# Kernel tuning notes

Hardware: AMD Instinct MI355X
Metric: run time of the kernel (lower is better)

## Reference

```python
import jax, jax.numpy as jnp
import numpy as np

B, N, D, DK = 8, 2048, 1024, 64
GAMMA = 0.001

def setup_inputs() -> dict:
    key = jax.random.key(0)
    ks = jax.random.split(key, 6)
    x = jax.random.normal(ks[0], (B, N, D), dtype=jnp.float32)
    # nn.Linear weights are [out_features, in_features]; init std=gamma,
    # except fc1/fc2 (modules 4,5) which get std=1e-12 in the original.
    Wq = GAMMA * jax.random.normal(ks[1], (DK, D), dtype=jnp.float32)
    Wk = GAMMA * jax.random.normal(ks[2], (DK, D), dtype=jnp.float32)
    Wv = GAMMA * jax.random.normal(ks[3], (D, D), dtype=jnp.float32)
    W1 = 1e-12 * jax.random.normal(ks[4], (DK, D), dtype=jnp.float32)
    W2 = 1e-12 * jax.random.normal(ks[5], (D, DK), dtype=jnp.float32)
    return {"x": x, "Wq": Wq, "Wk": Wk, "Wv": Wv, "W1": W1, "W2": W2}

def reference(x, Wq, Wk, Wv, W1, W2):
    # Q,K: [B,N,DK]; V: [B,N,D]
    Q = jnp.einsum('bnd,kd->bnk', x, Wq)
    K = jnp.einsum('bnd,kd->bnk', x, Wk)
    V = jnp.einsum('bnd,ed->bne', x, Wv)
    # Linear (non-softmax) attention: (Q @ K^T) @ V
    scores = jnp.einsum('bnk,bmk->bnm', Q, K)      # [B,N,N]
    attention = jnp.einsum('bnm,bme->bne', scores, V)  # [B,N,D]
    x_skip = x + attention
    fc = jnp.einsum('bnd,kd->bnk', x_skip, W1)     # [B,N,DK]
    out = jnp.einsum('bnk,dk->bnd', fc, W2)        # [B,N,D]
    return out
```

## Files before the change

### kernel.cpp

```cpp
#include <hip/hip_runtime.h>

typedef __attribute__((ext_vector_type(8))) __bf16 bf16x8;
typedef __attribute__((ext_vector_type(4))) float f32x4;
typedef unsigned short u16;

#define MFMA16(a, b, c) __builtin_amdgcn_mfma_f32_16x16x32_bf16(a, b, c, 0, 0, 0)

__device__ __forceinline__ unsigned cvt2(float a, float b) {
    unsigned r;
    asm("v_cvt_pk_bf16_f32 %0, %1, %2" : "=v"(r) : "v"(a), "v"(b));
    return r;
}
__device__ __forceinline__ u16 cvt1(float a) { return (u16)cvt2(a, a); }
__device__ __forceinline__ float lo2f(unsigned p) { return __uint_as_float(p << 16); }
__device__ __forceinline__ float hi2f(unsigned p) { return __uint_as_float(p & 0xffff0000u); }

__device__ __forceinline__ bf16x8 frag(const u16* base, int rtile, int lane, int kofs) {
    return *(const bf16x8*)(base + (rtile + (lane & 15)) * 72 + kofs + (lane >> 4) * 8);
}

__global__ __launch_bounds__(512, 4) void qkf_kernel(
    const float* __restrict__ x, const float* __restrict__ Wq,
    const float* __restrict__ Wk, const float* __restrict__ W1,
    float* __restrict__ Qp, float* __restrict__ Kp, float* __restrict__ fcp)
{
    __shared__ __align__(16) u16 SM[6 * 4608];
    u16* Xh  = SM;
    u16* Xl  = SM + 4608;
    u16* Wqh = SM + 2 * 4608;
    u16* Wkh = SM + 3 * 4608;
    u16* W1h = SM + 4 * 4608;
    u16* W1l = SM + 5 * 4608;

    const int tid  = threadIdx.x;
    const int lane = tid & 63;
    const int wv   = tid >> 6;
    const int rt   = (wv & 3) * 16;
    const int ch2  = wv >> 2;
    const long row0 = (long)blockIdx.x * 64;
    const int kb   = blockIdx.y * 512;
    const long sOf = (long)blockIdx.y * 1048576;

    const f32x4 zero = {0.f, 0.f, 0.f, 0.f};
    f32x4 qa[2], ka[2], fa[2];
#pragma unroll
    for (int i = 0; i < 2; ++i) { qa[i] = zero; ka[i] = zero; fa[i] = zero; }

    const int sr = tid >> 4;
    const int sk = (tid & 15) * 4;

    float4 xv0[2], xv1[2], qv[2], kv[2], w1v[2];

#define LOAD_X(S, K0)                                                         \
    { _Pragma("unroll")                                                       \
      for (int i = 0; i < 2; ++i)                                             \
          xv##S[i] = *(const float4*)(x + (row0 + sr + i * 32) * 1024 + (K0) + sk); }
#define LOAD_W(K0)                                                            \
    { _Pragma("unroll")                                                       \
      for (int i = 0; i < 2; ++i) {                                           \
          int r = sr + i * 32;                                                \
          qv[i]  = *(const float4*)(Wq + (long)r * 1024 + (K0) + sk);         \
          kv[i]  = *(const float4*)(Wk + (long)r * 1024 + (K0) + sk);         \
          w1v[i] = *(const float4*)(W1 + (long)r * 1024 + (K0) + sk);         \
      } }
#define CONV(S)                                                               \
    { _Pragma("unroll")                                                       \
      for (int i = 0; i < 2; ++i) {                                           \
          int r = sr + i * 32;                                                \
          unsigned xh01 = cvt2(xv##S[i].x, xv##S[i].y);                       \
          unsigned xh23 = cvt2(xv##S[i].z, xv##S[i].w);                       \
          unsigned xl01 = cvt2(xv##S[i].x - lo2f(xh01), xv##S[i].y - hi2f(xh01)); \
          unsigned xl23 = cvt2(xv##S[i].z - lo2f(xh23), xv##S[i].w - hi2f(xh23)); \
          uint2 t;                                                            \
          t.x = xh01; t.y = xh23; *(uint2*)&Xh[r * 72 + sk] = t;              \
          t.x = xl01; t.y = xl23; *(uint2*)&Xl[r * 72 + sk] = t;              \
          t.x = cvt2(qv[i].x, qv[i].y); t.y = cvt2(qv[i].z, qv[i].w);         \
          *(uint2*)&Wqh[r * 72 + sk] = t;                                     \
          t.x = cvt2(kv[i].x, kv[i].y); t.y = cvt2(kv[i].z, kv[i].w);         \
          *(uint2*)&Wkh[r * 72 + sk] = t;                                     \
          unsigned wh01 = cvt2(w1v[i].x, w1v[i].y);                           \
          unsigned wh23 = cvt2(w1v[i].z, w1v[i].w);                           \
          unsigned wl01 = cvt2(w1v[i].x - lo2f(wh01), w1v[i].y - hi2f(wh01)); \
          unsigned wl23 = cvt2(w1v[i].z - lo2f(wh23), w1v[i].w - hi2f(wh23)); \
          t.x = wh01; t.y = wh23; *(uint2*)&W1h[r * 72 + sk] = t;             \
          t.x = wl01; t.y = wl23; *(uint2*)&W1l[r * 72 + sk] = t;             \
      } }
#define MFMA_PHASE                                                            \
    { _Pragma("unroll")                                                       \
      for (int kk = 0; kk < 64; kk += 32) {                                   \
          bf16x8 ah = frag(Xh, rt, lane, kk);                                 \
          bf16x8 al = frag(Xl, rt, lane, kk);                                 \
          _Pragma("unroll")                                                   \
          for (int c = 0; c < 2; ++c) {                                       \
              int ct = ch2 * 2 + c;                                           \
              qa[c] = MFMA16(ah, frag(Wqh, ct * 16, lane, kk), qa[c]);        \
              ka[c] = MFMA16(ah, frag(Wkh, ct * 16, lane, kk), ka[c]);        \
              bf16x8 bh = frag(W1h, ct * 16, lane, kk);                       \
              fa[c] = MFMA16(ah, bh, fa[c]);                                  \
              fa[c] = MFMA16(al, bh, fa[c]);                                  \
              fa[c] = MFMA16(ah, frag(W1l, ct * 16, lane, kk), fa[c]);        \
          }                                                                   \
      } }

    LOAD_X(0, kb) LOAD_X(1, kb + 64) LOAD_W(kb)

    for (int cp = 0; cp < 4; ++cp) {
        const int kc = kb + cp * 128;
        if (cp) __syncthreads();
        CONV(0)
        __syncthreads();
        if (cp < 3) LOAD_X(0, kc + 128)
        LOAD_W(kc + 64)
        MFMA_PHASE
        __syncthreads();
        CONV(1)
        __syncthreads();
        if (cp < 3) { LOAD_X(1, kc + 192) LOAD_W(kc + 128) }
        MFMA_PHASE
    }
#undef LOAD_X
#undef LOAD_W
#undef CONV
#undef MFMA_PHASE

    const int rr = rt + (lane >> 4) * 4;
    const int cc = lane & 15;
#pragma unroll
    for (int c = 0; c < 2; ++c)
#pragma unroll
        for (int g = 0; g < 4; ++g) {
            long o = sOf + (row0 + rr + g) * 64 + (ch2 * 2 + c) * 16 + cc;
            Qp[o]  = qa[c][g];
            Kp[o]  = ka[c][g];
            fcp[o] = fa[c][g];
        }
}

__global__ __launch_bounds__(256) void s_kernel(
    const float* __restrict__ Kp, const float* __restrict__ x,
    float* __restrict__ Sp)
{
    __shared__ __align__(16) u16 Kt[64 * 72];
    __shared__ __align__(16) u16 Xt[64 * 72];

    const int tid = threadIdx.x, lane = tid & 63, wv = tid >> 6;
    const int dt = blockIdx.x, ks = blockIdx.y, b = blockIdx.z;
    const int n0 = ks * 256, d0 = dt * 64;

    const float* Kq = Kp + ((long)b * 2048 + n0) * 64;
    const float* xp = x  + ((long)b * 2048 + n0) * 1024 + d0;

    const f32x4 zero = {0.f, 0.f, 0.f, 0.f};
    f32x4 acc[4];
#pragma unroll
    for (int i = 0; i < 4; ++i) acc[i] = zero;

    float4 kf[4], xv[4];
#define SK_LOAD(NB)                                                           \
    {                                                                         \
        _Pragma("unroll")                                                     \
        for (int i = 0; i < 4; ++i) {                                         \
            float4 a = *(const float4*)(Kq + (long)((NB) + lane) * 64 + wv * 16 + i * 4); \
            float4 c = *(const float4*)(Kq + 1048576 + (long)((NB) + lane) * 64 + wv * 16 + i * 4); \
            kf[i].x = a.x + c.x; kf[i].y = a.y + c.y;                         \
            kf[i].z = a.z + c.z; kf[i].w = a.w + c.w;                         \
            xv[i] = *(const float4*)(xp + (long)((NB) + lane) * 1024 + wv * 16 + i * 4); \
        }                                                                     \
    }

    SK_LOAD(0)
    for (int ch = 0; ch < 4; ++ch) {
        if (ch) __syncthreads();
#pragma unroll
        for (int i = 0; i < 4; ++i) {
            Kt[(wv * 16 + i * 4 + 0) * 72 + lane] = cvt1(kf[i].x);
            Kt[(wv * 16 + i * 4 + 1) * 72 + lane] = cvt1(kf[i].y);
            Kt[(wv * 16 + i * 4 + 2) * 72 + lane] = cvt1(kf[i].z);
            Kt[(wv * 16 + i * 4 + 3) * 72 + lane] = cvt1(kf[i].w);
            Xt[(wv * 16 + i * 4 + 0) * 72 + lane] = cvt1(xv[i].x);
            Xt[(wv * 16 + i * 4 + 1) * 72 + lane] = cvt1(xv[i].y);
            Xt[(wv * 16 + i * 4 + 2) * 72 + lane] = cvt1(xv[i].z);
            Xt[(wv * 16 + i * 4 + 3) * 72 + lane] = cvt1(xv[i].w);
        }
        __syncthreads();
        if (ch < 3) SK_LOAD((ch + 1) * 64)
#pragma unroll
        for (int kk = 0; kk < 64; kk += 32) {
            bf16x8 a = frag(Kt, wv * 16, lane, kk);
#pragma unroll
            for (int ct = 0; ct < 4; ++ct)
                acc[ct] = MFMA16(a, frag(Xt, ct * 16, lane, kk), acc[ct]);
        }
    }
#undef SK_LOAD

    float* C = Sp + ((long)ks * 8 + b) * 65536 + d0;
    const int rr = wv * 16 + (lane >> 4) * 4;
    const int cc = lane & 15;
#pragma unroll
    for (int ct = 0; ct < 4; ++ct)
#pragma unroll
        for (int g = 0; g < 4; ++g)
            C[(long)(rr + g) * 1024 + ct * 16 + cc] = acc[ct][g];
}

template <int AMODE, int BMODE, bool SPLIT, int ASLAB, int BSLAB, int CSLAB>
__global__ __launch_bounds__(256) void mm_nt(
    const void* __restrict__ Ap, int lda, long bsA, long slabA,
    const void* __restrict__ Bp, int ldb, long bsB, long slabB,
    float* __restrict__ Cp, int ldc, long bsC, long splitC,
    const float* __restrict__ Cin, long slabCin,
    int Kred, int nksplit)
{
    __shared__ __align__(16) u16 SMEM[(SPLIT ? 4 : 2) * 4608];
    u16* Ah = SMEM;
    u16* Bh = SMEM + 4608;
    u16* Al = SPLIT ? SMEM + 2 * 4608 : nullptr;
    u16* Bl = SPLIT ? SMEM + 3 * 4608 : nullptr;

    const int tid = threadIdx.x, lane = tid & 63, wv = tid >> 6;
    const int bm = blockIdx.x, bn = blockIdx.y;
    const int batch = blockIdx.z / nksplit;
    const int ks = blockIdx.z % nksplit;
    const int Kper = Kred / nksplit;
    const long kOff = (long)ks * Kper;

    const int r4 = tid >> 4, k4 = (tid & 15) * 4;
    const int r8 = tid >> 3, k8 = (tid & 7) * 8;

    const f32x4 zero = {0.f, 0.f, 0.f, 0.f};
    f32x4 acc[4];
#pragma unroll
    for (int i = 0; i < 4; ++i) acc[i] = zero;

    float4 fva[4], fvb[4];
    uint4  uva[2], uvb[2];
    float  tvb[16];

#define MM_LOADA(K0)                                                          \
    if constexpr (AMODE == 0) {                                               \
        const float* A = (const float*)Ap + (long)batch * bsA                 \
                       + (long)bm * 64 * lda + (K0);                          \
        _Pragma("unroll")                                                     \
        for (int i = 0; i < 4; ++i) {                                         \
            const float* p = A + (long)(r4 + i * 16) * lda + k4;              \
            float4 v = *(const float4*)p;                                     \
            _Pragma("unroll")                                                 \
            for (int s = 1; s < ASLAB; ++s) {                                 \
                float4 w = *(const float4*)(p + (long)s * slabA);             \
                v.x += w.x; v.y += w.y; v.z += w.z; v.w += w.w;               \
            }                                                                 \
            fva[i] = v;                                                       \
        }                                                                     \
    } else {                                                                  \
        const u16* A = (const u16*)Ap + (long)batch * bsA                     \
                     + (long)bm * 64 * lda + (K0);                            \
        _Pragma("unroll")                                                     \
        for (int i = 0; i < 2; ++i)                                           \
            uva[i] = *(const uint4*)(A + (long)(r8 + i * 32) * lda + k8);     \
    }
#define MM_LOADB(K0)                                                          \
    if constexpr (BMODE == 0) {                                               \
        const float* Bq = (const float*)Bp + (long)batch * bsB                \
                        + (long)bn * 64 * ldb + (K0);                         \
        _Pragma("unroll")                                                     \
        for (int i = 0; i < 4; ++i) {                                         \
            const float* p = Bq + (long)(r4 + i * 16) * ldb + k4;             \
            float4 v = *(const float4*)p;                                     \
            _Pragma("unroll")                                                 \
            for (int s = 1; s < BSLAB; ++s) {                                 \
                float4 w = *(const float4*)(p + (long)s * slabB);             \
                v.x += w.x; v.y += w.y; v.z += w.z; v.w += w.w;               \
            }                                                                 \
            fvb[i] = v;                                                       \
        }                                                                     \
    } else if constexpr (BMODE == 1) {                                        \
        const u16* Bq = (const u16*)Bp + (long)batch * bsB                    \
                      + (long)bn * 64 * ldb + (K0);                           \
        _Pragma("unroll")                                                     \
        for (int i = 0; i < 2; ++i)                                           \
            uvb[i] = *(const uint4*)(Bq + (long)(r8 + i * 32) * ldb + k8);    \
    } else {                                                                  \
        const float* Bq = (const float*)Bp + (long)batch * bsB                \
                        + (long)(K0) * ldb + (long)bn * 64;                   \
        _Pragma("unroll")                                                     \
        for (int i = 0; i < 16; ++i)                                          \
            tvb[i] = Bq[(long)((tid >> 6) + i * 4) * ldb + (tid & 63)];       \
    }

    MM_LOADA(kOff) MM_LOADB(kOff)
    for (int k0 = 0; k0 < Kper; k0 += 64) {
        if (k0) __syncthreads();
        if constexpr (AMODE == 0) {
#pragma unroll
            for (int i = 0; i < 4; ++i) {
                int r = r4 + i * 16;
                unsigned h01 = cvt2(fva[i].x, fva[i].y);
                unsigned h23 = cvt2(fva[i].z, fva[i].w);
                uint2 t; t.x = h01; t.y = h23;
                *(uint2*)&Ah[r * 72 + k4] = t;
                if constexpr (SPLIT) {
                    t.x = cvt2(fva[i].x - lo2f(h01), fva[i].y - hi2f(h01));
                    t.y = cvt2(fva[i].z - lo2f(h23), fva[i].w - hi2f(h23));
                    *(uint2*)&Al[r * 72 + k4] = t;
                }
            }
        } else {
#pragma unroll
            for (int i = 0; i < 2; ++i)
                *(uint4*)&Ah[(r8 + i * 32) * 72 + k8] = uva[i];
        }
        if constexpr (BMODE == 0) {
#pragma unroll
            for (int i = 0; i < 4; ++i) {
                int r = r4 + i * 16;
                unsigned h01 = cvt2(fvb[i].x, fvb[i].y);
                unsigned h23 = cvt2(fvb[i].z, fvb[i].w);
                uint2 t; t.x = h01; t.y = h23;
                *(uint2*)&Bh[r * 72 + k4] = t;
                if constexpr (SPLIT) {
                    t.x = cvt2(fvb[i].x - lo2f(h01), fvb[i].y - hi2f(h01));
                    t.y = cvt2(fvb[i].z - lo2f(h23), fvb[i].w - hi2f(h23));
                    *(uint2*)&Bl[r * 72 + k4] = t;
                }
            }
        } else if constexpr (BMODE == 1) {
#pragma unroll
            for (int i = 0; i < 2; ++i)
                *(uint4*)&Bh[(r8 + i * 32) * 72 + k8] = uvb[i];
        } else {
#pragma unroll
            for (int i = 0; i < 16; ++i)
                Bh[(tid & 63) * 72 + (tid >> 6) + i * 4] = cvt1(tvb[i]);
        }
        __syncthreads();
        if (k0 + 64 < Kper) { MM_LOADA(kOff + k0 + 64) MM_LOADB(kOff + k0 + 64) }
#pragma unroll
        for (int kk = 0; kk < 64; kk += 32) {
            bf16x8 ah = frag(Ah, wv * 16, lane, kk);
            bf16x8 al;
            if constexpr (SPLIT) al = frag(Al, wv * 16, lane, kk);
#pragma unroll
            for (int ct = 0; ct < 4; ++ct) {
                bf16x8 bh = frag(Bh, ct * 16, lane, kk);
                acc[ct] = MFMA16(ah, bh, acc[ct]);
                if constexpr (SPLIT) {
                    acc[ct] = MFMA16(al, bh, acc[ct]);
                    acc[ct] = MFMA16(ah, frag(Bl, ct * 16, lane, kk), acc[ct]);
                }
            }
        }
    }
#undef MM_LOADA
#undef MM_LOADB

    const long coff = (long)batch * bsC + (long)bm * 64 * ldc + (long)bn * 64;
    float* C = Cp + coff + (long)ks * splitC;
    const int rr = wv * 16 + (lane >> 4) * 4;
    const int cc = lane & 15;
#pragma unroll
    for (int ct = 0; ct < 4; ++ct)
#pragma unroll
        for (int g = 0; g < 4; ++g) {
            long idx = (long)(rr + g) * ldc + ct * 16 + cc;
            float v = acc[ct][g];
            if constexpr (CSLAB > 0) {
                const float* Ci = Cin + coff + idx;
#pragma unroll
                for (int s = 0; s < CSLAB; ++s) v += Ci[(long)s * slabCin];
            }
            C[idx] = v;
        }
}

extern "C" void kernel_launch(void* const* d_in, const int* in_sizes, int n_in,
                              void* d_out, int out_size, void* d_ws, size_t ws_size,
                              hipStream_t stream)
{
    const float* x  = (const float*)d_in[0];
    const float* Wq = (const float*)d_in[1];
    const float* Wk = (const float*)d_in[2];
    const float* Wv = (const float*)d_in[3];
    const float* W1 = (const float*)d_in[4];
    const float* W2 = (const float*)d_in[5];
    float* out = (float*)d_out;

    const size_t QPB = 8388608, KPB = 8388608, FCPB = 8388608,
                 SPB = 16777216, GPB = 2097152, PBB = 2097152, FCB = 4194304;
    const size_t need = QPB + KPB + FCPB + SPB + GPB + PBB + FCB;

    float *Qp, *Kp, *fcp, *Sp, *Gp, *PBp, *fcb;
    if (ws_size >= need) {
        char* w = (char*)d_ws;
        Qp  = (float*)w;  w += QPB;
        Kp  = (float*)w;  w += KPB;
        fcp = (float*)w;  w += FCPB;
        Sp  = (float*)w;  w += SPB;
        Gp  = (float*)w;  w += GPB;
        PBp = (float*)w;  w += PBB;
        fcb = (float*)w;
    } else {
        char* o = (char*)d_out;
        Qp  = (float*)o;  o += QPB;
        Kp  = (float*)o;  o += KPB;
        fcp = (float*)o;  o += FCPB;
        Sp  = (float*)o;  o += SPB;
        Gp  = (float*)o;  o += GPB;
        PBp = (float*)o;
        fcb = (float*)d_ws;
    }

    qkf_kernel<<<dim3(256, 2), 512, 0, stream>>>(x, Wq, Wk, W1, Qp, Kp, fcp);

    s_kernel<<<dim3(16, 8, 8), 256, 0, stream>>>(Kp, x, Sp);

    mm_nt<0, 2, false, 1, 1, 0><<<dim3(1, 16, 8), 256, 0, stream>>>(
        W1, 1024, 0, 0,   Wv, 1024, 0, 0,
        Gp, 1024, 0, 65536L, nullptr, 0, 1024, 8);

    mm_nt<0, 0, false, 8, 8, 0><<<dim3(1, 1, 128), 256, 0, stream>>>(
        Gp, 1024, 0, 65536L,   Sp, 1024, 65536L, 524288L,
        PBp, 64, 4096L, 32768L, nullptr, 0, 1024, 16);

    mm_nt<0, 0, false, 2, 16, 2><<<dim3(32, 1, 8), 256, 0, stream>>>(
        Qp, 64, 131072L, 1048576L,   PBp, 64, 4096L, 32768L,
        fcb, 64, 131072L, 0, fcp, 1048576L, 64, 1);

    mm_nt<0, 0, true, 1, 1, 0><<<dim3(256, 16, 1), 256, 0, stream>>>(
        fcb, 64, 0, 0,   W2, 64, 0, 0,
        out, 1024, 0, 0, nullptr, 0, 64, 1);
}
```

Measured before the change: 209.0 us.

## Retile QKF projection with 32x32 MFMA, swizzled LDS and 4-way K split

Rewrites the Q/K/fc1 projection kernel to use 128-row tiles with 32x32x16 bf16 MFMAs, XOR-swizzled unpadded LDS layouts, and a single-stage register prefetch. The K dimension split goes from 2 to 4 partial slabs, giving more blocks. Downstream consumers (s_kernel and the fc-combining GEMM) now sum four partials instead of two, and the workspace layout is enlarged to match. The aim is better MFMA efficiency and fewer LDS bank conflicts. The cost is doubled partial-sum traffic and larger workspace use.

```diff
diff --git a/kernel.cpp b/kernel.cpp
--- a/kernel.cpp
+++ b/kernel.cpp
@@ -2,9 +2,11 @@
 
 typedef __attribute__((ext_vector_type(8))) __bf16 bf16x8;
 typedef __attribute__((ext_vector_type(4))) float f32x4;
+typedef __attribute__((ext_vector_type(16))) float f32x16;
 typedef unsigned short u16;
 
 #define MFMA16(a, b, c) __builtin_amdgcn_mfma_f32_16x16x32_bf16(a, b, c, 0, 0, 0)
+#define MFMA32(a, b, c) __builtin_amdgcn_mfma_f32_32x32x16_bf16(a, b, c, 0, 0, 0)
 
 __device__ __forceinline__ unsigned cvt2(float a, float b) {
     unsigned r;
@@ -18,122 +20,125 @@
 __device__ __forceinline__ bf16x8 frag(const u16* base, int rtile, int lane, int kofs) {
     return *(const bf16x8*)(base + (rtile + (lane & 15)) * 72 + kofs + (lane >> 4) * 8);
 }
-
-__global__ __launch_bounds__(512, 4) void qkf_kernel(
+__device__ __forceinline__ bf16x8 frag32(const u16* base, int rtile, int lane, int kofs) {
+    int row = rtile + (lane & 31);
+    int ks  = kofs + (lane >> 5) * 8;
+    return *(const bf16x8*)(base + row * 64 + (ks ^ ((row & 7) << 3)));
+}
+
+__global__ __launch_bounds__(256, 2) void qkf_kernel(
     const float* __restrict__ x, const float* __restrict__ Wq,
     const float* __restrict__ Wk, const float* __restrict__ W1,
     float* __restrict__ Qp, float* __restrict__ Kp, float* __restrict__ fcp)
 {
-    __shared__ __align__(16) u16 SM[6 * 4608];
+    __shared__ __align__(16) u16 SM[32768];
     u16* Xh  = SM;
-    u16* Xl  = SM + 4608;
-    u16* Wqh = SM + 2 * 4608;
-    u16* Wkh = SM + 3 * 4608;
-    u16* W1h = SM + 4 * 4608;
-    u16* W1l = SM + 5 * 4608;
+    u16* Xl  = SM + 8192;
+    u16* Wqh = SM + 16384;
+    u16* Wkh = SM + 20480;
+    u16* W1h = SM + 24576;
+    u16* W1l = SM + 28672;
 
     const int tid  = threadIdx.x;
     const int lane = tid & 63;
     const int wv   = tid >> 6;
-    const int rt   = (wv & 3) * 16;
-    const int ch2  = wv >> 2;
-    const long row0 = (long)blockIdx.x * 64;
-    const int kb   = blockIdx.y * 512;
+    const int rh   = wv >> 1;
+    const int ch   = wv & 1;
+    const long row0 = (long)blockIdx.x * 128;
+    const int kb   = blockIdx.y * 256;
     const long sOf = (long)blockIdx.y * 1048576;
 
-    const f32x4 zero = {0.f, 0.f, 0.f, 0.f};
-    f32x4 qa[2], ka[2], fa[2];
-#pragma unroll
-    for (int i = 0; i < 2; ++i) { qa[i] = zero; ka[i] = zero; fa[i] = zero; }
-
-    const int sr = tid >> 4;
-    const int sk = (tid & 15) * 4;
-
-    float4 xv0[2], xv1[2], qv[2], kv[2], w1v[2];
-
-#define LOAD_X(S, K0)                                                         \
+    f32x16 qa0 = {}, qa1 = {}, ka0 = {}, ka1 = {}, fa0 = {}, fa1 = {};
+
+    const int sxr = tid >> 1;
+    const int sxk = (tid & 1) * 32;
+    const int xsw = (sxr & 7) << 3;
+    const int swr = tid >> 2;
+    const int swk = (tid & 3) * 16;
+    const int wsw = (swr & 7) << 3;
+
+    float4 xv[8], qv[4], kv[4], w1v[4];
+
+#define LOAD_X(K0)                                                            \
     { _Pragma("unroll")                                                       \
-      for (int i = 0; i < 2; ++i)                                             \
-          xv##S[i] = *(const float4*)(x + (row0 + sr + i * 32) * 1024 + (K0) + sk); }
+      for (int i = 0; i < 8; ++i)                                             \
+          xv[i] = *(const float4*)(x + (row0 + sxr) * 1024 + (K0) + sxk + i * 4); }
 #define LOAD_W(K0)                                                            \
     { _Pragma("unroll")                                                       \
-      for (int i = 0; i < 2; ++i) {                                           \
-          int r = sr + i * 32;                                                \
-          qv[i]  = *(const float4*)(Wq + (long)r * 1024 + (K0) + sk);         \
-          kv[i]  = *(const float4*)(Wk + (long)r * 1024 + (K0) + sk);         \
-          w1v[i] = *(const float4*)(W1 + (long)r * 1024 + (K0) + sk);         \
+      for (int i = 0; i < 4; ++i) {                                           \
+          qv[i]  = *(const float4*)(Wq + (long)swr * 1024 + (K0) + swk + i * 4); \
+          kv[i]  = *(const float4*)(Wk + (long)swr * 1024 + (K0) + swk + i * 4); \
+          w1v[i] = *(const float4*)(W1 + (long)swr * 1024 + (K0) + swk + i * 4); \
       } }
-#define CONV(S)                                                               \
+#define STAGE_X                                                               \
     { _Pragma("unroll")                                                       \
-      for (int i = 0; i < 2; ++i) {                                           \
-          int r = sr + i * 32;                                                \
-          unsigned xh01 = cvt2(xv##S[i].x, xv##S[i].y);                       \
-          unsigned xh23 = cvt2(xv##S[i].z, xv##S[i].w);                       \
-          unsigned xl01 = cvt2(xv##S[i].x - lo2f(xh01), xv##S[i].y - hi2f(xh01)); \
-          unsigned xl23 = cvt2(xv##S[i].z - lo2f(xh23), xv##S[i].w - hi2f(xh23)); \
+      for (int i = 0; i < 8; ++i) {                                           \
+          int o = sxr * 64 + ((sxk + i * 4) ^ xsw);                           \
+          unsigned h01 = cvt2(xv[i].x, xv[i].y);                              \
+          unsigned h23 = cvt2(xv[i].z, xv[i].w);                              \
+          unsigned l01 = cvt2(xv[i].x - lo2f(h01), xv[i].y - hi2f(h01));      \
+          unsigned l23 = cvt2(xv[i].z - lo2f(h23), xv[i].w - hi2f(h23));      \
+          uint2 t; t.x = h01; t.y = h23; *(uint2*)&Xh[o] = t;                 \
+          t.x = l01; t.y = l23; *(uint2*)&Xl[o] = t;                          \
+      } }
+#define STAGE_W                                                               \
+    { _Pragma("unroll")                                                       \
+      for (int i = 0; i < 4; ++i) {                                           \
+          int o = swr * 64 + ((swk + i * 4) ^ wsw);                           \
           uint2 t;                                                            \
-          t.x = xh01; t.y = xh23; *(uint2*)&Xh[r * 72 + sk] = t;              \
-          t.x = xl01; t.y = xl23; *(uint2*)&Xl[r * 72 + sk] = t;              \
           t.x = cvt2(qv[i].x, qv[i].y); t.y = cvt2(qv[i].z, qv[i].w);         \
-          *(uint2*)&Wqh[r * 72 + sk] = t;                                     \
+          *(uint2*)&Wqh[o] = t;                                               \
           t.x = cvt2(kv[i].x, kv[i].y); t.y = cvt2(kv[i].z, kv[i].w);         \
-          *(uint2*)&Wkh[r * 72 + sk] = t;                                     \
-          unsigned wh01 = cvt2(w1v[i].x, w1v[i].y);                           \
-          unsigned wh23 = cvt2(w1v[i].z, w1v[i].w);                           \
-          unsigned wl01 = cvt2(w1v[i].x - lo2f(wh01), w1v[i].y - hi2f(wh01)); \
-          unsigned wl23 = cvt2(w1v[i].z - lo2f(wh23), w1v[i].w - hi2f(wh23)); \
-          t.x = wh01; t.y = wh23; *(uint2*)&W1h[r * 72 + sk] = t;             \
-          t.x = wl01; t.y = wl23; *(uint2*)&W1l[r * 72 + sk] = t;             \
+          *(uint2*)&Wkh[o] = t;                                               \
+          unsigned h01 = cvt2(w1v[i].x, w1v[i].y);                            \
+          unsigned h23 = cvt2(w1v[i].z, w1v[i].w);                            \
+          t.x = h01; t.y = h23; *(uint2*)&W1h[o] = t;                         \
+          t.x = cvt2(w1v[i].x - lo2f(h01), w1v[i].y - hi2f(h01));             \
+          t.y = cvt2(w1v[i].z - lo2f(h23), w1v[i].w - hi2f(h23));             \
+          *(uint2*)&W1l[o] = t;                                               \
       } }
-#define MFMA_PHASE                                                            \
-    { _Pragma("unroll")                                                       \
-      for (int kk = 0; kk < 64; kk += 32) {                                   \
-          bf16x8 ah = frag(Xh, rt, lane, kk);                                 \
-          bf16x8 al = frag(Xl, rt, lane, kk);                                 \
-          _Pragma("unroll")                                                   \
-          for (int c = 0; c < 2; ++c) {                                       \
-              int ct = ch2 * 2 + c;                                           \
-              qa[c] = MFMA16(ah, frag(Wqh, ct * 16, lane, kk), qa[c]);        \
-              ka[c] = MFMA16(ah, frag(Wkh, ct * 16, lane, kk), ka[c]);        \
-              bf16x8 bh = frag(W1h, ct * 16, lane, kk);                       \
-              fa[c] = MFMA16(ah, bh, fa[c]);                                  \
-              fa[c] = MFMA16(al, bh, fa[c]);                                  \
-              fa[c] = MFMA16(ah, frag(W1l, ct * 16, lane, kk), fa[c]);        \
-          }                                                                   \
-      } }
-
-    LOAD_X(0, kb) LOAD_X(1, kb + 64) LOAD_W(kb)
-
-    for (int cp = 0; cp < 4; ++cp) {
-        const int kc = kb + cp * 128;
-        if (cp) __syncthreads();
-        CONV(0)
+
+    LOAD_X(kb) LOAD_W(kb)
+    for (int c = 0; c < 4; ++c) {
+        if (c) __syncthreads();
+        STAGE_X
+        STAGE_W
         __syncthreads();
-        if (cp < 3) LOAD_X(0, kc + 128)
-        LOAD_W(kc + 64)
-        MFMA_PHASE
-        __syncthreads();
-        CONV(1)
-        __syncthreads();
-        if (cp < 3) { LOAD_X(1, kc + 192) LOAD_W(kc + 128) }
-        MFMA_PHASE
+        if (c < 3) { LOAD_X(kb + (c + 1) * 64) LOAD_W(kb + (c + 1) * 64) }
+#pragma unroll
+        for (int s = 0; s < 4; ++s) {
+            const int ko = s * 16;
+            bf16x8 xh0 = frag32(Xh, rh * 64,      lane, ko);
+            bf16x8 xh1 = frag32(Xh, rh * 64 + 32, lane, ko);
+            bf16x8 xl0 = frag32(Xl, rh * 64,      lane, ko);
+            bf16x8 xl1 = frag32(Xl, rh * 64 + 32, lane, ko);
+            bf16x8 bq  = frag32(Wqh, ch * 32, lane, ko);
+            bf16x8 bk  = frag32(Wkh, ch * 32, lane, ko);
+            bf16x8 b1h = frag32(W1h, ch * 32, lane, ko);
+            bf16x8 b1l = frag32(W1l, ch * 32, lane, ko);
+            qa0 = MFMA32(xh0, bq, qa0);   qa1 = MFMA32(xh1, bq, qa1);
+            ka0 = MFMA32(xh0, bk, ka0);   ka1 = MFMA32(xh1, bk, ka1);
+            fa0 = MFMA32(xh0, b1h, fa0);  fa1 = MFMA32(xh1, b1h, fa1);
+            fa0 = MFMA32(xl0, b1h, fa0);  fa1 = MFMA32(xl1, b1h, fa1);
+            fa0 = MFMA32(xh0, b1l, fa0);  fa1 = MFMA32(xh1, b1l, fa1);
+        }
     }
 #undef LOAD_X
 #undef LOAD_W
-#undef CONV
-#undef MFMA_PHASE
-
-    const int rr = rt + (lane >> 4) * 4;
-    const int cc = lane & 15;
-#pragma unroll
-    for (int c = 0; c < 2; ++c)
-#pragma unroll
-        for (int g = 0; g < 4; ++g) {
-            long o = sOf + (row0 + rr + g) * 64 + (ch2 * 2 + c) * 16 + cc;
-            Qp[o]  = qa[c][g];
-            Kp[o]  = ka[c][g];
-            fcp[o] = fa[c][g];
-        }
+#undef STAGE_X
+#undef STAGE_W
+
+    const int col = lane & 31;
+    const int rb  = (lane >> 5) * 4;
+#pragma unroll
+    for (int g = 0; g < 16; ++g) {
+        int r = (g & 3) + 8 * (g >> 2) + rb;
+        long o0 = sOf + (row0 + rh * 64 + r) * 64 + ch * 32 + col;
+        long o1 = o0 + 32 * 64;
+        Qp[o0]  = qa0[g];  Qp[o1]  = qa1[g];
+        Kp[o0]  = ka0[g];  Kp[o1]  = ka1[g];
+        fcp[o0] = fa0[g];  fcp[o1] = fa1[g];
+    }
 }
 
 __global__ __launch_bounds__(256) void s_kernel(
@@ -160,10 +165,15 @@
     {                                                                         \
         _Pragma("unroll")                                                     \
         for (int i = 0; i < 4; ++i) {                                         \
-            float4 a = *(const float4*)(Kq + (long)((NB) + lane) * 64 + wv * 16 + i * 4); \
-            float4 c = *(const float4*)(Kq + 1048576 + (long)((NB) + lane) * 64 + wv * 16 + i * 4); \
-            kf[i].x = a.x + c.x; kf[i].y = a.y + c.y;                         \
-            kf[i].z = a.z + c.z; kf[i].w = a.w + c.w;                         \
+            long off = (long)((NB) + lane) * 64 + wv * 16 + i * 4;            \
+            float4 a0 = *(const float4*)(Kq + off);                           \
+            float4 a1 = *(const float4*)(Kq + 1048576 + off);                 \
+            float4 a2 = *(const float4*)(Kq + 2097152 + off);                 \
+            float4 a3 = *(const float4*)(Kq + 3145728 + off);                 \
+            kf[i].x = (a0.x + a1.x) + (a2.x + a3.x);                          \
+            kf[i].y = (a0.y + a1.y) + (a2.y + a3.y);                          \
+            kf[i].z = (a0.z + a1.z) + (a2.z + a3.z);                          \
+            kf[i].w = (a0.w + a1.w) + (a2.w + a3.w);                          \
             xv[i] = *(const float4*)(xp + (long)((NB) + lane) * 1024 + wv * 16 + i * 4); \
         }                                                                     \
     }
@@ -385,7 +395,7 @@
     const float* W2 = (const float*)d_in[5];
     float* out = (float*)d_out;
 
-    const size_t QPB = 8388608, KPB = 8388608, FCPB = 8388608,
+    const size_t QPB = 16777216, KPB = 16777216, FCPB = 16777216,
                  SPB = 16777216, GPB = 2097152, PBB = 2097152, FCB = 4194304;
     const size_t need = QPB + KPB + FCPB + SPB + GPB + PBB + FCB;
 
@@ -404,13 +414,14 @@
         Qp  = (float*)o;  o += QPB;
         Kp  = (float*)o;  o += KPB;
         fcp = (float*)o;  o += FCPB;
-        Sp  = (float*)o;  o += SPB;
-        Gp  = (float*)o;  o += GPB;
-        PBp = (float*)o;
-        fcb = (float*)d_ws;
-    }
-
-    qkf_kernel<<<dim3(256, 2), 512, 0, stream>>>(x, Wq, Wk, W1, Qp, Kp, fcp);
+        Sp  = (float*)o;
+        char* w = (char*)d_ws;
+        Gp  = (float*)w;  w += GPB;
+        PBp = (float*)w;  w += PBB;
+        fcb = (float*)w;
+    }
+
+    qkf_kernel<<<dim3(128, 4), 256, 0, stream>>>(x, Wq, Wk, W1, Qp, Kp, fcp);
 
     s_kernel<<<dim3(16, 8, 8), 256, 0, stream>>>(Kp, x, Sp);
 
@@ -422,7 +433,7 @@
         Gp, 1024, 0, 65536L,   Sp, 1024, 65536L, 524288L,
         PBp, 64, 4096L, 32768L, nullptr, 0, 1024, 16);
 
-    mm_nt<0, 0, false, 2, 16, 2><<<dim3(32, 1, 8), 256, 0, stream>>>(
+    mm_nt<0, 0, false, 4, 16, 4><<<dim3(32, 1, 8), 256, 0, stream>>>(
         Qp, 64, 131072L, 1048576L,   PBp, 64, 4096L, 32768L,
         fcb, 64, 131072L, 0, fcp, 1048576L, 64, 1);
 
```

After: 238.1 us. 13.9% more time.

## Pre-reduce K split halves to bf16 and double-buffer s_kernel loads

Applied to the files above, without the earlier changes.

Adds a small kernel that sums the two split-K partials of K once and stores the result as bf16, so s_kernel reads half-width K instead of re-reading and summing two fp32 copies in each of its 16 d-tile blocks. s_kernel also gains a two-deep register prefetch (loads two chunks ahead) to hide global latency behind MFMA work. The cost is an extra kernel launch and workspace buffer, plus higher register pressure from the doubled staging registers.

```diff
diff --git a/kernel.cpp b/kernel.cpp
--- a/kernel.cpp
+++ b/kernel.cpp
@@ -136,8 +136,24 @@
         }
 }
 
+__global__ __launch_bounds__(256) void ksum_kernel(
+    const float* __restrict__ Kp, u16* __restrict__ Kb)
+{
+    const long g = ((long)blockIdx.x * 256 + threadIdx.x) * 8;
+    float4 a0 = *(const float4*)(Kp + g);
+    float4 a1 = *(const float4*)(Kp + g + 4);
+    float4 b0 = *(const float4*)(Kp + 1048576 + g);
+    float4 b1 = *(const float4*)(Kp + 1048576 + g + 4);
+    uint4 r;
+    r.x = cvt2(a0.x + b0.x, a0.y + b0.y);
+    r.y = cvt2(a0.z + b0.z, a0.w + b0.w);
+    r.z = cvt2(a1.x + b1.x, a1.y + b1.y);
+    r.w = cvt2(a1.z + b1.z, a1.w + b1.w);
+    *(uint4*)(Kb + g) = r;
+}
+
 __global__ __launch_bounds__(256) void s_kernel(
-    const float* __restrict__ Kp, const float* __restrict__ x,
+    const u16* __restrict__ Kb, const float* __restrict__ x,
     float* __restrict__ Sp)
 {
     __shared__ __align__(16) u16 Kt[64 * 72];
@@ -147,7 +163,7 @@
     const int dt = blockIdx.x, ks = blockIdx.y, b = blockIdx.z;
     const int n0 = ks * 256, d0 = dt * 64;
 
-    const float* Kq = Kp + ((long)b * 2048 + n0) * 64;
+    const u16*   Kq = Kb + ((long)b * 2048 + n0) * 64;
     const float* xp = x  + ((long)b * 2048 + n0) * 1024 + d0;
 
     const f32x4 zero = {0.f, 0.f, 0.f, 0.f};
@@ -155,35 +171,39 @@
 #pragma unroll
     for (int i = 0; i < 4; ++i) acc[i] = zero;
 
-    float4 kf[4], xv[4];
-#define SK_LOAD(NB)                                                           \
-    {                                                                         \
-        _Pragma("unroll")                                                     \
-        for (int i = 0; i < 4; ++i) {                                         \
-            float4 a = *(const float4*)(Kq + (long)((NB) + lane) * 64 + wv * 16 + i * 4); \
-            float4 c = *(const float4*)(Kq + 1048576 + (long)((NB) + lane) * 64 + wv * 16 + i * 4); \
-            kf[i].x = a.x + c.x; kf[i].y = a.y + c.y;                         \
-            kf[i].z = a.z + c.z; kf[i].w = a.w + c.w;                         \
-            xv[i] = *(const float4*)(xp + (long)((NB) + lane) * 1024 + wv * 16 + i * 4); \
-        }                                                                     \
-    }
-
-    SK_LOAD(0)
+    uint2  ku0[4], ku1[4];
+    float4 xv0[4], xv1[4];
+
+#define SK_LOAD(S, NB)                                                        \
+    { _Pragma("unroll")                                                       \
+      for (int i = 0; i < 4; ++i) {                                           \
+          ku##S[i] = *(const uint2*)(Kq + (long)((NB) + lane) * 64 + wv * 16 + i * 4); \
+          xv##S[i] = *(const float4*)(xp + (long)((NB) + lane) * 1024 + wv * 16 + i * 4); \
+      } }
+#define SK_STAGE(S)                                                           \
+    { _Pragma("unroll")                                                       \
+      for (int i = 0; i < 4; ++i) {                                           \
+          int r = wv * 16 + i * 4;                                            \
+          Kt[(r + 0) * 72 + lane] = (u16)(ku##S[i].x);                        \
+          Kt[(r + 1) * 72 + lane] = (u16)(ku##S[i].x >> 16);                  \
+          Kt[(r + 2) * 72 + lane] = (u16)(ku##S[i].y);                        \
+          Kt[(r + 3) * 72 + lane] = (u16)(ku##S[i].y >> 16);                  \
+          Xt[(r + 0) * 72 + lane] = cvt1(xv##S[i].x);                         \
+          Xt[(r + 1) * 72 + lane] = cvt1(xv##S[i].y);                         \
+          Xt[(r + 2) * 72 + lane] = cvt1(xv##S[i].z);                         \
+          Xt[(r + 3) * 72 + lane] = cvt1(xv##S[i].w);                         \
+      } }
+
+    SK_LOAD(0, 0) SK_LOAD(1, 64)
+#pragma unroll
     for (int ch = 0; ch < 4; ++ch) {
         if (ch) __syncthreads();
-#pragma unroll
-        for (int i = 0; i < 4; ++i) {
-            Kt[(wv * 16 + i * 4 + 0) * 72 + lane] = cvt1(kf[i].x);
-            Kt[(wv * 16 + i * 4 + 1) * 72 + lane] = cvt1(kf[i].y);
-            Kt[(wv * 16 + i * 4 + 2) * 72 + lane] = cvt1(kf[i].z);
-            Kt[(wv * 16 + i * 4 + 3) * 72 + lane] = cvt1(kf[i].w);
-            Xt[(wv * 16 + i * 4 + 0) * 72 + lane] = cvt1(xv[i].x);
-            Xt[(wv * 16 + i * 4 + 1) * 72 + lane] = cvt1(xv[i].y);
-            Xt[(wv * 16 + i * 4 + 2) * 72 + lane] = cvt1(xv[i].z);
-            Xt[(wv * 16 + i * 4 + 3) * 72 + lane] = cvt1(xv[i].w);
-        }
+        if (ch & 1) { SK_STAGE(1) } else { SK_STAGE(0) }
         __syncthreads();
-        if (ch < 3) SK_LOAD((ch + 1) * 64)
+        if (ch < 2) {
+            if (ch & 1) { SK_LOAD(1, (ch + 2) * 64) }
+            else        { SK_LOAD(0, (ch + 2) * 64) }
+        }
 #pragma unroll
         for (int kk = 0; kk < 64; kk += 32) {
             bf16x8 a = frag(Kt, wv * 16, lane, kk);
@@ -193,6 +213,7 @@
         }
     }
 #undef SK_LOAD
+#undef SK_STAGE
 
     float* C = Sp + ((long)ks * 8 + b) * 65536 + d0;
     const int rr = wv * 16 + (lane >> 4) * 4;
@@ -386,10 +407,12 @@
     float* out = (float*)d_out;
 
     const size_t QPB = 8388608, KPB = 8388608, FCPB = 8388608,
-                 SPB = 16777216, GPB = 2097152, PBB = 2097152, FCB = 4194304;
-    const size_t need = QPB + KPB + FCPB + SPB + GPB + PBB + FCB;
+                 SPB = 16777216, GPB = 2097152, PBB = 2097152, FCB = 4194304,
+                 KBFB = 2097152;
+    const size_t need = QPB + KPB + FCPB + SPB + GPB + PBB + FCB + KBFB;
 
     float *Qp, *Kp, *fcp, *Sp, *Gp, *PBp, *fcb;
+    u16* Kbf;
     if (ws_size >= need) {
         char* w = (char*)d_ws;
         Qp  = (float*)w;  w += QPB;
@@ -398,7 +421,8 @@
         Sp  = (float*)w;  w += SPB;
         Gp  = (float*)w;  w += GPB;
         PBp = (float*)w;  w += PBB;
-        fcb = (float*)w;
+        fcb = (float*)w;  w += FCB;
+        Kbf = (u16*)w;
     } else {
         char* o = (char*)d_out;
         Qp  = (float*)o;  o += QPB;
@@ -406,13 +430,16 @@
         fcp = (float*)o;  o += FCPB;
         Sp  = (float*)o;  o += SPB;
         Gp  = (float*)o;  o += GPB;
-        PBp = (float*)o;
+        PBp = (float*)o;  o += PBB;
+        Kbf = (u16*)o;
         fcb = (float*)d_ws;
     }
 
     qkf_kernel<<<dim3(256, 2), 512, 0, stream>>>(x, Wq, Wk, W1, Qp, Kp, fcp);
 
-    s_kernel<<<dim3(16, 8, 8), 256, 0, stream>>>(Kp, x, Sp);
+    ksum_kernel<<<512, 256, 0, stream>>>(Kp, Kbf);
+
+    s_kernel<<<dim3(16, 8, 8), 256, 0, stream>>>(Kbf, x, Sp);
 
     mm_nt<0, 2, false, 1, 1, 0><<<dim3(1, 16, 8), 256, 0, stream>>>(
         W1, 1024, 0, 0,   Wv, 1024, 0, 0,
```

After: 199.0 us. 4.8% less time.
